# Optimization experiments

Hardware: AMD Instinct MI355X
Metric: run time of the kernel (lower is better)

The kernel has to match this reference:

```python
import jax, jax.numpy as jnp
import numpy as np
from jax import lax

B, D = 512, 256
C = 10  # hidden conv channels


def setup_inputs() -> dict:
    key = jax.random.key(0)
    ks = jax.random.split(key, 9)
    x = jax.random.normal(ks[0], (B, D, D), jnp.float32)
    w1 = jax.random.normal(ks[1], (C, 1, 1, 1), jnp.float32) * 0.1   # Conv2d(1,10,1)
    b1 = jax.random.normal(ks[2], (C,), jnp.float32) * 0.01
    w2 = jax.random.normal(ks[3], (1, C, 3, 3), jnp.float32) * 0.05  # Conv2d(10,1,3,1,1)
    b2 = jax.random.normal(ks[4], (1,), jnp.float32) * 0.01
    fc1_w = jax.random.normal(ks[5], (4, D * B), jnp.float32) * (1.0 / np.sqrt(D * B))
    fc1_b = jax.random.normal(ks[6], (4,), jnp.float32) * 0.01
    fc2_w = jax.random.normal(ks[7], (2, 4), jnp.float32) * 0.5
    fc2_b = jax.random.normal(ks[8], (2,), jnp.float32) * 0.01
    return {"x": x, "w1": w1, "b1": b1, "w2": w2, "b2": b2,
            "fc1_w": fc1_w, "fc1_b": fc1_b, "fc2_w": fc2_w, "fc2_b": fc2_b}


def reference(x, w1, b1, w2, b2, fc1_w, fc1_b, fc2_w, fc2_b):
    # edge-to-edge: E[b,i,j] = row_sum(i) + col_sum(j)
    rs = x.sum(axis=-1)          # [B, D]
    cs = x.sum(axis=-2)          # [B, D]
    e = (rs[:, :, None] + cs[:, None, :])[:, None]  # [B, 1, D, D]
    # Conv2d(1, C, 1) == per-pixel scale+bias over channels
    h = jax.nn.relu(e * w1.reshape(1, C, 1, 1) + b1.reshape(1, C, 1, 1))  # [B, C, D, D]
    # convSym: lower-triangular mask each channel
    h = h * jnp.tril(jnp.ones((D, D), jnp.float32))
    # Conv2d(C, 1, 3, stride=1, pad=1)
    y = lax.conv_general_dilated(h, w2, (1, 1), 'SAME',
                                 dimension_numbers=('NCHW', 'OIHW', 'NCHW'))
    y = jax.nn.relu(y + b2.reshape(1, 1, 1, 1))[:, 0]  # [B, D, D]
    # edge-to-vertex: v[b,i] = row_sum + col_sum
    v = y.sum(axis=-1) + y.sum(axis=-2)  # [B, D]
    flat = v.reshape(-1)                  # [B*D]
    hfc = jax.nn.relu(fc1_w @ flat + fc1_b)
    return fc2_w @ hfc + fc2_b            # [2]
```

## Files before the change

### kernel.cpp

```cpp
#include <hip/hip_runtime.h>

#define DD 256
#define BB 512
#define NL 2048

#define OFF_RS   0
#define OFF_CSP  131072
#define OFF_HFC  655360
#define OFF_PAR  655368
#define OFF_TABP 655376
#define OFF_LUT  655648

__device__ __forceinline__ float wave_red(float v) {
#pragma unroll
  for (int off = 32; off > 0; off >>= 1) v += __shfl_down(v, off, 64);
  return v;
}

__global__ void ktab_kernel(const float* __restrict__ w1, const float* __restrict__ b1,
                            const float* __restrict__ w2, float* __restrict__ ws) {
  const int t = threadIdx.x;
  float w1v[10], b1v[10], bp[10];
  int rank[10];
#pragma unroll
  for (int c = 0; c < 10; ++c) { w1v[c] = w1[c]; b1v[c] = b1[c]; bp[c] = -b1v[c] / w1v[c]; }
#pragma unroll
  for (int c = 0; c < 10; ++c) {
    int r = 0;
#pragma unroll
    for (int k = 0; k < 10; ++k)
      r += (bp[k] < bp[c] || (bp[k] == bp[c] && k < c)) ? 1 : 0;
    rank[c] = r;
  }
  float lo = bp[0], hi = bp[0];
#pragma unroll
  for (int c = 1; c < 10; ++c) { lo = fminf(lo, bp[c]); hi = fmaxf(hi, bp[c]); }
  const float step = (hi - lo) / (float)(NL - 3);
  if (t == 0) {
    ws[OFF_PAR]     = (float)(NL - 3) / (hi - lo);
    ws[OFF_PAR + 1] = 1.0f - lo * ((float)(NL - 3) / (hi - lo));
  }
  if (t < 99) {
    const int s = t / 9, tt = t % 9;
    const int dr = tt / 3, kc = tt % 3;
    float A = 0.f, Bv = 0.f;
    for (int c = 0; c < 10; ++c) {
      bool act = (w1v[c] > 0.f) ? (rank[c] < s)
               : ((w1v[c] < 0.f) ? (rank[c] >= s) : (b1v[c] > 0.f));
      if (act) { A += w1v[c] * w2[c * 9 + tt]; Bv += b1v[c] * w2[c * 9 + tt]; }
    }
    ws[OFF_TABP + (s * 3 + kc) * 8 + dr * 2]     = A;
    ws[OFF_TABP + (s * 3 + kc) * 8 + dr * 2 + 1] = Bv;
  }
  unsigned short* lut = (unsigned short*)(ws + OFF_LUT);
  for (int k = t; k < NL; k += 256) {
    const float x = lo + (float)(k - 1) * step;
    int s = 0;
#pragma unroll
    for (int c = 0; c < 10; ++c) s += (bp[c] < x) ? 1 : 0;
    lut[k] = (unsigned short)(s * 96);
  }
}

__global__ __launch_bounds__(256) void sum_kernel(const float* __restrict__ x,
                                                  float* __restrict__ ws) {
  const int bq = blockIdx.x;
  const int b = bq >> 2;
  const int q = bq & 3;
  const int tid = threadIdx.x;
  const int lane = tid & 63;
  const int wv = tid >> 6;
  __shared__ float rowp[64][65];
  __shared__ float csl[4][DD];
  __shared__ float segp[4][64];
  float4 cacc = make_float4(0.f, 0.f, 0.f, 0.f);
  const float4* px = (const float4*)(x + ((size_t)b << 16) + ((size_t)(q * 64 + wv * 16) << 8));
#pragma unroll
  for (int r = 0; r < 16; ++r) {
    float4 val = px[r * 64 + lane];
    cacc.x += val.x; cacc.y += val.y; cacc.z += val.z; cacc.w += val.w;
    rowp[wv * 16 + r][lane] = (val.x + val.y) + (val.z + val.w);
  }
  ((float4*)csl[wv])[lane] = cacc;
  __syncthreads();
  {
    const int row = tid & 63, seg = tid >> 6;
    const float* rp = rowp[row] + seg * 16;
    float s = 0.f;
#pragma unroll
    for (int k = 0; k < 16; ++k) s += rp[k];
    segp[seg][row] = s;
  }
  __syncthreads();
  if (tid < 64)
    ws[OFF_RS + b * DD + q * 64 + tid] =
        (segp[0][tid] + segp[1][tid]) + (segp[2][tid] + segp[3][tid]);
  ws[OFF_CSP + bq * DD + tid] =
      (csl[0][tid] + csl[1][tid]) + (csl[2][tid] + csl[3][tid]);
  if (bq == 0 && tid < 4) ws[OFF_HFC + tid] = 0.f;
}

__global__ __launch_bounds__(1024, 8) void conv_kernel(const float* __restrict__ b2p,
                                                       const float* __restrict__ fc1w,
                                                       float* __restrict__ ws) {
  const int b = blockIdx.x;
  const int tid = threadIdx.x;
  const int w = tid >> 6;
  const int lane = tid & 63;
  const int q = w >> 2;
  const int wb = (w - q) & 3;
  const int seg = q;
  const int j = wb * 64 + lane;
  const int jmin = wb * 64;
  const int r0 = seg * 64, r1 = r0 + 64;

  __shared__ __align__(16) float tabP[264];
  __shared__ float rs_s[DD];
  __shared__ float cs_s[DD];
  __shared__ __align__(16) float wkA[DD][4];
  __shared__ unsigned short lut_s[NL];
  __shared__ float segsum_s[4][4];
  __shared__ float red_s[64];

  ((unsigned int*)lut_s)[tid] = ((const unsigned int*)(ws + OFF_LUT))[tid];
  if (tid < 256) {
    rs_s[tid] = ws[OFF_RS + b * DD + tid];
  } else if (tid < 512) {
    const int t = tid - 256;
    const float* csp = ws + OFF_CSP + (b * 4) * DD + t;
    cs_s[t] = (csp[0] + csp[DD]) + (csp[2 * DD] + csp[3 * DD]);
  } else if (tid < 768) {
    const int r = tid - 512;
#pragma unroll
    for (int k = 0; k < 4; ++k) wkA[r][k] = fc1w[k * (BB * DD) + b * DD + r];
  } else {
    const int u = tid - 768;
    if (u < 256) tabP[u] = ws[OFF_TABP + u];
  }
  if (tid < 8) tabP[256 + tid] = ws[OFF_TABP + 256 + tid];
  __syncthreads();
  if (tid < 16) {
    const int ss = tid >> 2, k = tid & 3;
    float s = 0.f;
#pragma unroll
    for (int r = 0; r < 64; ++r) s += wkA[ss * 64 + r][k];
    segsum_s[ss][k] = s;
  }
  __syncthreads();

  const float inv_step = ws[OFF_PAR];
  const float bias = ws[OFF_PAR + 1];
  const float b2v = b2p[0];
  const float yb = fmaxf(b2v, 0.f);

  float csr[3], vf[3];
  csr[0] = (j >= 1) ? cs_s[j - 1] : 0.f;
  csr[1] = cs_s[j];
  csr[2] = (j < DD - 1) ? cs_s[j + 1] : 0.f;
  vf[0] = (j >= 1) ? 1.f : 0.f;
  vf[1] = 1.f;
  vf[2] = (j < DD - 1) ? 1.f : 0.f;

  const int nt = min(max(jmin - 2 - r0, 0), 64);
  const int rfirst = r0 + nt;
  const int ibeg = (nt > 0) ? rfirst - 1 : ((r0 == 0) ? 0 : r0 - 1);
  const int iend = (r1 == DD) ? DD - 1 : r1;
  const int ffrom = rfirst + 1;

  float P = 0.f, Q = 0.f;
  float vcol = 64.f * yb;
  float acc0 = yb * segsum_s[seg][0];
  float acc1 = yb * segsum_s[seg][1];
  float acc2 = yb * segsum_s[seg][2];
  float acc3 = yb * segsum_s[seg][3];

  if (rfirst < r1) {
    for (int i = ibeg; i <= iend; ++i) {
      const float rsv = rs_s[i];
      float R0 = 0.f, R1 = 0.f, R2 = 0.f;
      if (j - 1 <= i) {
#pragma unroll
        for (int kc = 0; kc < 3; ++kc) {
          const float e = rsv + csr[kc];
          float fx = fmaf(e, inv_step, bias);
          fx = fminf(fmaxf(fx, 0.f), (float)(NL - 1));
          const int off = (int)lut_s[(int)fx];
          const char* tp = (const char*)tabP + (off + kc * 32);
          const float4 ab01 = *(const float4*)tp;
          const float2 ab2  = *(const float2*)(tp + 16);
          const float m = ((j - 1 + kc) <= i) ? vf[kc] : 0.f;
          R0 = fmaf(m, fmaf(ab01.x, e, ab01.y), R0);
          R1 = fmaf(m, fmaf(ab01.z, e, ab01.w), R1);
          R2 = fmaf(m, fmaf(ab2.x, e, ab2.y), R2);
        }
      }
      if (i >= ffrom) {
        const float yd = fmaxf(P + R2 + b2v, 0.f) - yb;
        vcol += yd;
        const float4 wkv = *(const float4*)wkA[i - 1];
        acc0 = fmaf(yd, wkv.x, acc0);
        acc1 = fmaf(yd, wkv.y, acc1);
        acc2 = fmaf(yd, wkv.z, acc2);
        acc3 = fmaf(yd, wkv.w, acc3);
      }
      P = Q + R1;
      Q = R0;
    }
  }
  if (r1 == DD) {
    const float yd = fmaxf(P + b2v, 0.f) - yb;
    vcol += yd;
    const float4 wkv = *(const float4*)wkA[DD - 1];
    acc0 = fmaf(yd, wkv.x, acc0);
    acc1 = fmaf(yd, wkv.y, acc1);
    acc2 = fmaf(yd, wkv.z, acc2);
    acc3 = fmaf(yd, wkv.w, acc3);
  }

  const float4 wkj = *(const float4*)wkA[j];
  acc0 = fmaf(vcol, wkj.x, acc0);
  acc1 = fmaf(vcol, wkj.y, acc1);
  acc2 = fmaf(vcol, wkj.z, acc2);
  acc3 = fmaf(vcol, wkj.w, acc3);

  acc0 = wave_red(acc0); acc1 = wave_red(acc1);
  acc2 = wave_red(acc2); acc3 = wave_red(acc3);
  if (lane == 0) {
    red_s[w * 4 + 0] = acc0; red_s[w * 4 + 1] = acc1;
    red_s[w * 4 + 2] = acc2; red_s[w * 4 + 3] = acc3;
  }
  __syncthreads();
  if (tid < 4) {
    float s = 0.f;
#pragma unroll
    for (int wv = 0; wv < 16; ++wv) s += red_s[wv * 4 + tid];
    atomicAdd(&ws[OFF_HFC + tid], s);
  }
}

__global__ void fc_kernel(const float* __restrict__ fc1b, const float* __restrict__ fc2w,
                          const float* __restrict__ fc2b, const float* __restrict__ ws,
                          float* __restrict__ out) {
  if (threadIdx.x == 0 && blockIdx.x == 0) {
    float o0 = fc2b[0], o1 = fc2b[1];
#pragma unroll
    for (int k = 0; k < 4; ++k) {
      float h = fmaxf(ws[OFF_HFC + k] + fc1b[k], 0.f);
      o0 += fc2w[k] * h;
      o1 += fc2w[4 + k] * h;
    }
    out[0] = o0; out[1] = o1;
  }
}

extern "C" void kernel_launch(void* const* d_in, const int* in_sizes, int n_in,
                              void* d_out, int out_size, void* d_ws, size_t ws_size,
                              hipStream_t stream) {
  const float* x    = (const float*)d_in[0];
  const float* w1   = (const float*)d_in[1];
  const float* b1   = (const float*)d_in[2];
  const float* w2   = (const float*)d_in[3];
  const float* b2   = (const float*)d_in[4];
  const float* fc1w = (const float*)d_in[5];
  const float* fc1b = (const float*)d_in[6];
  const float* fc2w = (const float*)d_in[7];
  const float* fc2b = (const float*)d_in[8];
  float* out = (float*)d_out;
  float* ws  = (float*)d_ws;

  hipLaunchKernelGGL(ktab_kernel, dim3(1), dim3(256), 0, stream, w1, b1, w2, ws);
  hipLaunchKernelGGL(sum_kernel,  dim3(2048), dim3(256), 0, stream, x, ws);
  hipLaunchKernelGGL(conv_kernel, dim3(512), dim3(1024), 0, stream, b2, fc1w, ws);
  hipLaunchKernelGGL(fc_kernel,   dim3(1), dim3(64), 0, stream, fc1b, fc2w, fc2b, ws, out);
}
```

Before: 249.7 us.

## Fold table setup into sum kernel, pack conv taps into float2 FMAs, split loops

```diff
diff --git a/kernel.cpp b/kernel.cpp
--- a/kernel.cpp
+++ b/kernel.cpp
@@ -11,63 +11,82 @@
 #define OFF_TABP 655376
 #define OFF_LUT  655648
 
+typedef float v2f __attribute__((ext_vector_type(2)));
+
+__device__ __forceinline__ v2f mk2(float a, float b) { v2f r; r.x = a; r.y = b; return r; }
+
+__device__ __forceinline__ v2f fma2(v2f a, v2f b, v2f c) {
+#if __has_builtin(__builtin_elementwise_fma)
+  return __builtin_elementwise_fma(a, b, c);
+#else
+  return mk2(fmaf(a.x, b.x, c.x), fmaf(a.y, b.y, c.y));
+#endif
+}
+
 __device__ __forceinline__ float wave_red(float v) {
 #pragma unroll
   for (int off = 32; off > 0; off >>= 1) v += __shfl_down(v, off, 64);
   return v;
 }
 
-__global__ void ktab_kernel(const float* __restrict__ w1, const float* __restrict__ b1,
-                            const float* __restrict__ w2, float* __restrict__ ws) {
-  const int t = threadIdx.x;
-  float w1v[10], b1v[10], bp[10];
-  int rank[10];
-#pragma unroll
-  for (int c = 0; c < 10; ++c) { w1v[c] = w1[c]; b1v[c] = b1[c]; bp[c] = -b1v[c] / w1v[c]; }
-#pragma unroll
-  for (int c = 0; c < 10; ++c) {
-    int r = 0;
-#pragma unroll
-    for (int k = 0; k < 10; ++k)
-      r += (bp[k] < bp[c] || (bp[k] == bp[c] && k < c)) ? 1 : 0;
-    rank[c] = r;
-  }
-  float lo = bp[0], hi = bp[0];
-#pragma unroll
-  for (int c = 1; c < 10; ++c) { lo = fminf(lo, bp[c]); hi = fmaxf(hi, bp[c]); }
-  const float step = (hi - lo) / (float)(NL - 3);
-  if (t == 0) {
-    ws[OFF_PAR]     = (float)(NL - 3) / (hi - lo);
-    ws[OFF_PAR + 1] = 1.0f - lo * ((float)(NL - 3) / (hi - lo));
-  }
-  if (t < 99) {
-    const int s = t / 9, tt = t % 9;
-    const int dr = tt / 3, kc = tt % 3;
-    float A = 0.f, Bv = 0.f;
-    for (int c = 0; c < 10; ++c) {
-      bool act = (w1v[c] > 0.f) ? (rank[c] < s)
-               : ((w1v[c] < 0.f) ? (rank[c] >= s) : (b1v[c] > 0.f));
-      if (act) { A += w1v[c] * w2[c * 9 + tt]; Bv += b1v[c] * w2[c * 9 + tt]; }
-    }
-    ws[OFF_TABP + (s * 3 + kc) * 8 + dr * 2]     = A;
-    ws[OFF_TABP + (s * 3 + kc) * 8 + dr * 2 + 1] = Bv;
-  }
-  unsigned short* lut = (unsigned short*)(ws + OFF_LUT);
-  for (int k = t; k < NL; k += 256) {
-    const float x = lo + (float)(k - 1) * step;
-    int s = 0;
-#pragma unroll
-    for (int c = 0; c < 10; ++c) s += (bp[c] < x) ? 1 : 0;
-    lut[k] = (unsigned short)(s * 96);
-  }
-}
-
 __global__ __launch_bounds__(256) void sum_kernel(const float* __restrict__ x,
+                                                  const float* __restrict__ w1,
+                                                  const float* __restrict__ b1,
+                                                  const float* __restrict__ w2,
                                                   float* __restrict__ ws) {
   const int bq = blockIdx.x;
+  const int tid = threadIdx.x;
+  if (bq == 2048) {
+    const int t = tid;
+    float w1v[10], b1v[10], bp[10];
+    int rank[10];
+#pragma unroll
+    for (int c = 0; c < 10; ++c) { w1v[c] = w1[c]; b1v[c] = b1[c]; bp[c] = -b1v[c] / w1v[c]; }
+#pragma unroll
+    for (int c = 0; c < 10; ++c) {
+      int r = 0;
+#pragma unroll
+      for (int k = 0; k < 10; ++k)
+        r += (bp[k] < bp[c] || (bp[k] == bp[c] && k < c)) ? 1 : 0;
+      rank[c] = r;
+    }
+    float lo = bp[0], hi = bp[0];
+#pragma unroll
+    for (int c = 1; c < 10; ++c) { lo = fminf(lo, bp[c]); hi = fmaxf(hi, bp[c]); }
+    const float step = (hi - lo) / (float)(NL - 3);
+    if (t == 0) {
+      ws[OFF_PAR]     = (float)(NL - 3) / (hi - lo);
+      ws[OFF_PAR + 1] = 1.0f - lo * ((float)(NL - 3) / (hi - lo));
+    }
+    if (t < 99) {
+      const int s = t / 9, tt = t % 9;
+      const int dr = tt / 3, kc = tt % 3;
+      float A = 0.f, Bv = 0.f;
+      for (int c = 0; c < 10; ++c) {
+        bool act = (w1v[c] > 0.f) ? (rank[c] < s)
+                 : ((w1v[c] < 0.f) ? (rank[c] >= s) : (b1v[c] > 0.f));
+        if (act) { A += w1v[c] * w2[c * 9 + tt]; Bv += b1v[c] * w2[c * 9 + tt]; }
+      }
+      const int base = (s * 3 + kc) * 8;
+      const int posA = (dr == 2) ? 4 : dr;
+      const int posB = (dr == 2) ? 5 : (2 + dr);
+      ws[OFF_TABP + base + posA] = A;
+      ws[OFF_TABP + base + posB] = Bv;
+      ws[OFF_TABP + base + 6] = 0.f;
+      ws[OFF_TABP + base + 7] = 0.f;
+    }
+    unsigned short* lut = (unsigned short*)(ws + OFF_LUT);
+    for (int k = t; k < NL; k += 256) {
+      const float xx = lo + (float)(k - 1) * step;
+      int s = 0;
+#pragma unroll
+      for (int c = 0; c < 10; ++c) s += (bp[c] < xx) ? 1 : 0;
+      lut[k] = (unsigned short)(s * 96);
+    }
+    return;
+  }
   const int b = bq >> 2;
   const int q = bq & 3;
-  const int tid = threadIdx.x;
   const int lane = tid & 63;
   const int wv = tid >> 6;
   __shared__ float rowp[64][65];
@@ -107,9 +126,8 @@
   const int tid = threadIdx.x;
   const int w = tid >> 6;
   const int lane = tid & 63;
-  const int q = w >> 2;
-  const int wb = (w - q) & 3;
-  const int seg = q;
+  const int seg = w >> 2;
+  const int wb = (w - seg) & 3;
   const int j = wb * 64 + lane;
   const int jmin = wb * 64;
   const int r0 = seg * 64, r1 = r0 + 64;
@@ -152,6 +170,7 @@
   const float bias = ws[OFF_PAR + 1];
   const float b2v = b2p[0];
   const float yb = fmaxf(b2v, 0.f);
+  const float fxmax = (float)(NL - 1);
 
   float csr[3], vf[3];
   csr[0] = (j >= 1) ? cs_s[j - 1] : 0.f;
@@ -160,71 +179,99 @@
   vf[0] = (j >= 1) ? 1.f : 0.f;
   vf[1] = 1.f;
   vf[2] = (j < DD - 1) ? 1.f : 0.f;
+  v2f vf2[3];
+#pragma unroll
+  for (int kc = 0; kc < 3; ++kc) vf2[kc] = mk2(vf[kc], vf[kc]);
 
   const int nt = min(max(jmin - 2 - r0, 0), 64);
   const int rfirst = r0 + nt;
-  const int ibeg = (nt > 0) ? rfirst - 1 : ((r0 == 0) ? 0 : r0 - 1);
   const int iend = (r1 == DD) ? DD - 1 : r1;
-  const int ffrom = rfirst + 1;
 
   float P = 0.f, Q = 0.f;
   float vcol = 64.f * yb;
-  float acc0 = yb * segsum_s[seg][0];
-  float acc1 = yb * segsum_s[seg][1];
-  float acc2 = yb * segsum_s[seg][2];
-  float acc3 = yb * segsum_s[seg][3];
+  v2f a01 = mk2(yb * segsum_s[seg][0], yb * segsum_s[seg][1]);
+  v2f a23 = mk2(yb * segsum_s[seg][2], yb * segsum_s[seg][3]);
+
+#define TAP_CORE(KC, E, M2, MS)                                              \
+  {                                                                          \
+    float fx = fmaf((E), inv_step, bias);                                    \
+    fx = fminf(fmaxf(fx, 0.f), fxmax);                                       \
+    const int off = (int)lut_s[(int)fx];                                     \
+    const char* tp = (const char*)tabP + (off + (KC) * 32);                  \
+    const float4 ab = *(const float4*)tp;                   \
+    const float2 ab2 = *(const float2*)(tp + 16);                 \
+    v2f tv = fma2(mk2(ab.x, ab.y), mk2((E), (E)), mk2(ab.z, ab.w));          \
+    R01 = fma2((M2), tv, R01);                                               \
+    R2 = fmaf((MS), fmaf(ab2.x, (E), ab2.y), R2);                            \
+  }
 
   if (rfirst < r1) {
-    for (int i = ibeg; i <= iend; ++i) {
-      const float rsv = rs_s[i];
-      float R0 = 0.f, R1 = 0.f, R2 = 0.f;
-      if (j - 1 <= i) {
+    if (seg > wb) {
+      for (int i = r0 - 1; i <= r0; ++i) {
+        const float rsv = rs_s[i];
+        v2f R01 = mk2(0.f, 0.f); float R2 = 0.f;
 #pragma unroll
         for (int kc = 0; kc < 3; ++kc) {
           const float e = rsv + csr[kc];
-          float fx = fmaf(e, inv_step, bias);
-          fx = fminf(fmaxf(fx, 0.f), (float)(NL - 1));
-          const int off = (int)lut_s[(int)fx];
-          const char* tp = (const char*)tabP + (off + kc * 32);
-          const float4 ab01 = *(const float4*)tp;
-          const float2 ab2  = *(const float2*)(tp + 16);
           const float m = ((j - 1 + kc) <= i) ? vf[kc] : 0.f;
-          R0 = fmaf(m, fmaf(ab01.x, e, ab01.y), R0);
-          R1 = fmaf(m, fmaf(ab01.z, e, ab01.w), R1);
-          R2 = fmaf(m, fmaf(ab2.x, e, ab2.y), R2);
+          TAP_CORE(kc, e, mk2(m, m), m)
         }
+        P = Q + R01.y; Q = R01.x;
       }
-      if (i >= ffrom) {
+      for (int i = r0 + 1; i <= iend; ++i) {
+        const float rsv = rs_s[i];
+        v2f R01 = mk2(0.f, 0.f); float R2 = 0.f;
+#pragma unroll
+        for (int kc = 0; kc < 3; ++kc) {
+          const float e = rsv + csr[kc];
+          TAP_CORE(kc, e, vf2[kc], vf[kc])
+        }
         const float yd = fmaxf(P + R2 + b2v, 0.f) - yb;
         vcol += yd;
         const float4 wkv = *(const float4*)wkA[i - 1];
-        acc0 = fmaf(yd, wkv.x, acc0);
-        acc1 = fmaf(yd, wkv.y, acc1);
-        acc2 = fmaf(yd, wkv.z, acc2);
-        acc3 = fmaf(yd, wkv.w, acc3);
+        a01 = fma2(mk2(yd, yd), mk2(wkv.x, wkv.y), a01);
+        a23 = fma2(mk2(yd, yd), mk2(wkv.z, wkv.w), a23);
+        P = Q + R01.y; Q = R01.x;
       }
-      P = Q + R1;
-      Q = R0;
+    } else {
+      const int ibeg = (nt > 0) ? rfirst - 1 : ((r0 == 0) ? 0 : r0 - 1);
+      const int ffrom = rfirst + 1;
+      for (int i = ibeg; i <= iend; ++i) {
+        const float rsv = rs_s[i];
+        v2f R01 = mk2(0.f, 0.f); float R2 = 0.f;
+        if (j - 1 <= i) {
+#pragma unroll
+          for (int kc = 0; kc < 3; ++kc) {
+            const float e = rsv + csr[kc];
+            const float m = ((j - 1 + kc) <= i) ? vf[kc] : 0.f;
+            TAP_CORE(kc, e, mk2(m, m), m)
+          }
+        }
+        if (i >= ffrom) {
+          const float yd = fmaxf(P + R2 + b2v, 0.f) - yb;
+          vcol += yd;
+          const float4 wkv = *(const float4*)wkA[i - 1];
+          a01 = fma2(mk2(yd, yd), mk2(wkv.x, wkv.y), a01);
+          a23 = fma2(mk2(yd, yd), mk2(wkv.z, wkv.w), a23);
+        }
+        P = Q + R01.y; Q = R01.x;
+      }
     }
   }
   if (r1 == DD) {
     const float yd = fmaxf(P + b2v, 0.f) - yb;
     vcol += yd;
     const float4 wkv = *(const float4*)wkA[DD - 1];
-    acc0 = fmaf(yd, wkv.x, acc0);
-    acc1 = fmaf(yd, wkv.y, acc1);
-    acc2 = fmaf(yd, wkv.z, acc2);
-    acc3 = fmaf(yd, wkv.w, acc3);
+    a01 = fma2(mk2(yd, yd), mk2(wkv.x, wkv.y), a01);
+    a23 = fma2(mk2(yd, yd), mk2(wkv.z, wkv.w), a23);
   }
 
   const float4 wkj = *(const float4*)wkA[j];
-  acc0 = fmaf(vcol, wkj.x, acc0);
-  acc1 = fmaf(vcol, wkj.y, acc1);
-  acc2 = fmaf(vcol, wkj.z, acc2);
-  acc3 = fmaf(vcol, wkj.w, acc3);
-
-  acc0 = wave_red(acc0); acc1 = wave_red(acc1);
-  acc2 = wave_red(acc2); acc3 = wave_red(acc3);
+  a01 = fma2(mk2(vcol, vcol), mk2(wkj.x, wkj.y), a01);
+  a23 = fma2(mk2(vcol, vcol), mk2(wkj.z, wkj.w), a23);
+
+  float acc0 = wave_red(a01.x), acc1 = wave_red(a01.y);
+  float acc2 = wave_red(a23.x), acc3 = wave_red(a23.y);
   if (lane == 0) {
     red_s[w * 4 + 0] = acc0; red_s[w * 4 + 1] = acc1;
     red_s[w * 4 + 2] = acc2; red_s[w * 4 + 3] = acc3;
@@ -236,6 +283,7 @@
     for (int wv = 0; wv < 16; ++wv) s += red_s[wv * 4 + tid];
     atomicAdd(&ws[OFF_HFC + tid], s);
   }
+#undef TAP_CORE
 }
 
 __global__ void fc_kernel(const float* __restrict__ fc1b, const float* __restrict__ fc2w,
@@ -268,8 +316,7 @@
   float* out = (float*)d_out;
   float* ws  = (float*)d_ws;
 
-  hipLaunchKernelGGL(ktab_kernel, dim3(1), dim3(256), 0, stream, w1, b1, w2, ws);
-  hipLaunchKernelGGL(sum_kernel,  dim3(2048), dim3(256), 0, stream, x, ws);
+  hipLaunchKernelGGL(sum_kernel,  dim3(2049), dim3(256), 0, stream, x, w1, b1, w2, ws);
   hipLaunchKernelGGL(conv_kernel, dim3(512), dim3(1024), 0, stream, b2, fc1w, ws);
   hipLaunchKernelGGL(fc_kernel,   dim3(1), dim3(64), 0, stream, fc1b, fc2w, fc2b, ws, out);
 }
```

After: 243.2 us. 2.6% less time.
